# Optimization experiments

Measured on AMD Instinct MI355X. Metric: run time of the kernel, lower is better.

## Reference

```python
import jax, jax.numpy as jnp
import numpy as np

B, NF, E, A = 4096, 40, 64, 32  # batch, num feature fields, embedding_size, attention_size


def setup_inputs() -> dict:
    key = jax.random.key(0)
    kx, kw, kb, kh = jax.random.split(key, 4)
    return {
        "x": jax.random.normal(kx, (B, NF, E), dtype=jnp.float32),
        "W": jax.random.normal(kw, (E, A), dtype=jnp.float32) * 0.05,  # random_normal init
        "b": jax.random.normal(kb, (A,), dtype=jnp.float32) * 0.05,
        "h": jax.random.normal(kh, (A,), dtype=jnp.float32) * 0.05,
        "p": jnp.ones((E, 1), dtype=jnp.float32),  # 'ones' initializer
    }


def reference(x, W, b, h, p):
    nf = x.shape[1]
    # pairwise (i<j) element-wise products, same ordering as the double loop
    ii, jj = np.triu_indices(nf, k=1)
    ewp = x[:, ii, :] * x[:, jj, :]                      # (B, P, E), P = nf*(nf-1)/2
    # attention MLP: relu(ewp @ W + b) . h, then exp-normalize over pairs
    a = jax.nn.relu(jnp.einsum('bpe,ea->bpa', ewp, W) + b)  # (B, P, A)
    e = jnp.exp(jnp.sum(a * h, axis=-1))                 # (B, P)  (faithful: no max-subtract)
    att = e / jnp.sum(e, axis=1, keepdims=True)          # (B, P)
    pooled = jnp.einsum('bp,bpe->be', att, ewp)          # attention-weighted sum over pairs
    return pooled @ p                                    # (B, 1)
```

## Files before the change

kernel.cpp:

```cpp
#include <hip/hip_runtime.h>

#define NFEAT 40
#define EMB   64
#define ATT   32
#define NPAIR 780
#define NMT   49
#define XH_S  72

typedef __attribute__((ext_vector_type(8))) _Float16 f16x8;
typedef __attribute__((ext_vector_type(4))) _Float16 f16x4;
typedef __attribute__((ext_vector_type(4))) float    f32x4;

template <int CTRL>
__device__ __forceinline__ float dpp_add_f(float v) {
  int t = __builtin_amdgcn_update_dpp(0, __float_as_int(v), CTRL, 0xF, 0xF, true);
  return v + __int_as_float(t);
}
__device__ __forceinline__ float rowsum16(float v) {
  v = dpp_add_f<0x128>(v);
  v = dpp_add_f<0x124>(v);
  v = dpp_add_f<0x122>(v);
  v = dpp_add_f<0x121>(v);
  return v;
}

__device__ __forceinline__ int pair_off(int i) { return 39 * i - (i * (i - 1)) / 2; }

extern "C" __global__ __launch_bounds__(256)
void afm_kernel(const float* __restrict__ xg, const float* __restrict__ Wg,
                const float* __restrict__ bg, const float* __restrict__ hg,
                const float* __restrict__ pg, float* __restrict__ outg, int nbatch) {
  __shared__ __align__(16) _Float16 xh[NFEAT * XH_S];
  __shared__ float red[4][2];

  const int tid  = threadIdx.x;
  const int lane = tid & 63, wid = tid >> 6;
  const int l15  = lane & 15, hk = lane >> 4;

  f16x8 wf0[2], wf1[2], wf2[2];
#pragma unroll
  for (int kk = 0; kk < 2; kk++) {
    f16x8 r0, r1, r2;
#pragma unroll
    for (int t = 0; t < 8; t++) {
      int krow = kk * 32 + hk * 8 + t;
      r0[t] = (_Float16)Wg[krow * ATT + l15];
      r1[t] = (_Float16)Wg[krow * ATT + 16 + l15];
      _Float16 pv = (_Float16)pg[krow];
      r2[t] = (l15 == 0) ? pv : (_Float16)0.f;
    }
    wf0[kk] = r0; wf1[kk] = r1; wf2[kk] = r2;
  }
  const float4 b0 = *(const float4*)&bg[hk * 4];
  const float4 b1 = *(const float4*)&bg[16 + hk * 4];
  const float4 h0 = *(const float4*)&hg[hk * 4];
  const float4 h1 = *(const float4*)&hg[16 + hk * 4];

  unsigned pij[13];
#pragma unroll
  for (int t = 0; t < 13; t++) {
    int p = (wid + 4 * t) * 16 + l15;
    int i = 0, j = 0;
    if (p < NPAIR) {
      i = (int)((79.0f - sqrtf(6241.0f - 8.0f * (float)p)) * 0.5f);
      if (i < 0) i = 0;
      while (pair_off(i + 1) <= p) ++i;
      while (pair_off(i) > p) --i;
      j = i + 1 + (p - pair_off(i));
    }
    pij[t] = (unsigned)(i * 144 + hk * 16) | ((unsigned)(j * 144 + hk * 16) << 16);
  }

  const f32x4 kz = {0.f, 0.f, 0.f, 0.f};

  for (int it = 0; it < 2; it++) {
    const int bb = blockIdx.x * 2 + it;
    if (bb >= nbatch) break;

    const float4* xsrc = (const float4*)(xg + (size_t)bb * (NFEAT * EMB));
    for (int f = tid; f < NFEAT * EMB / 4; f += 256) {
      float4 v = xsrc[f];
      int row = f >> 4, c = (f & 15) * 4;
      f16x4 h4 = {(_Float16)v.x, (_Float16)v.y, (_Float16)v.z, (_Float16)v.w};
      *(f16x4*)&xh[row * XH_S + c] = h4;
    }
    __syncthreads();

    float sum_e = 0.f, sum_es = 0.f;
#pragma unroll
    for (int t = 0; t < 13; t++) {
      if (t < 12 || wid == 0) {
        const unsigned offi = pij[t] & 0xFFFFu;
        const unsigned offj = pij[t] >> 16;
        const f16x8 xi0 = *(const f16x8*)((const char*)xh + offi);
        const f16x8 xj0 = *(const f16x8*)((const char*)xh + offj);
        const f16x8 xi1 = *(const f16x8*)((const char*)xh + offi + 64);
        const f16x8 xj1 = *(const f16x8*)((const char*)xh + offj + 64);
        f16x8 af0 = xi0 * xj0;
        f16x8 af1 = xi1 * xj1;
        f32x4 acc0 = __builtin_amdgcn_mfma_f32_16x16x32_f16(wf0[0], af0, kz, 0, 0, 0);
        f32x4 acc1 = __builtin_amdgcn_mfma_f32_16x16x32_f16(wf1[0], af0, kz, 0, 0, 0);
        f32x4 acc2 = __builtin_amdgcn_mfma_f32_16x16x32_f16(wf2[0], af0, kz, 0, 0, 0);
        acc0 = __builtin_amdgcn_mfma_f32_16x16x32_f16(wf0[1], af1, acc0, 0, 0, 0);
        acc1 = __builtin_amdgcn_mfma_f32_16x16x32_f16(wf1[1], af1, acc1, 0, 0, 0);
        acc2 = __builtin_amdgcn_mfma_f32_16x16x32_f16(wf2[1], af1, acc2, 0, 0, 0);
        float va = fmaf(fmaxf(acc0[0] + b0.x, 0.f), h0.x,
                   fmaf(fmaxf(acc0[1] + b0.y, 0.f), h0.y,
                   fmaf(fmaxf(acc0[2] + b0.z, 0.f), h0.z,
                        fmaxf(acc0[3] + b0.w, 0.f) * h0.w)));
        float vb = fmaf(fmaxf(acc1[0] + b1.x, 0.f), h1.x,
                   fmaf(fmaxf(acc1[1] + b1.y, 0.f), h1.y,
                   fmaf(fmaxf(acc1[2] + b1.z, 0.f), h1.z,
                        fmaxf(acc1[3] + b1.w, 0.f) * h1.w)));
        float v = va + vb;
        v += __shfl_xor(v, 16, 64);
        v += __shfl_xor(v, 32, 64);
        float e = __expf(v);
        if (t == 12) e = (l15 < 12) ? e : 0.f;
        sum_e += e;
        sum_es = fmaf(e, acc2[0], sum_es);
      }
    }

    sum_e = rowsum16(sum_e);
    sum_e += __shfl_xor(sum_e, 16, 64);
    sum_e += __shfl_xor(sum_e, 32, 64);
    sum_es = rowsum16(sum_es);
    sum_es += __shfl_xor(sum_es, 16, 64);
    sum_es += __shfl_xor(sum_es, 32, 64);
    if (lane == 0) { red[wid][0] = sum_e; red[wid][1] = sum_es; }
    __syncthreads();
    if (tid == 0) {
      float Z = (red[0][0] + red[1][0] + red[2][0] + red[3][0]) * 0.25f;
      float S = red[0][1] + red[1][1] + red[2][1] + red[3][1];
      outg[bb] = S / Z;
    }
  }
}

extern "C" void kernel_launch(void* const* d_in, const int* in_sizes, int n_in,
                              void* d_out, int out_size, void* d_ws, size_t ws_size,
                              hipStream_t stream) {
  const float* xg = (const float*)d_in[0];
  const float* Wg = (const float*)d_in[1];
  const float* bg = (const float*)d_in[2];
  const float* hg = (const float*)d_in[3];
  const float* pg = (const float*)d_in[4];
  float* outg = (float*)d_out;
  const int Bn = in_sizes[0] / (NFEAT * EMB);
  const int nblk = (Bn + 1) / 2;
  afm_kernel<<<dim3(nblk), dim3(256), 0, stream>>>(xg, Wg, bg, hg, pg, outg, Bn);
}
```

Before: 39.82 us.

## Use single-wave blocks with LDS pair table and bias folded into MFMA

Each block now runs one 64-lane wave instead of four, and that wave loops over all 49 pair tiles per batch row. Per-lane pair offsets move from registers into a shared-memory table, and the bias is passed in as the MFMA accumulator init. The cross-wave shared reduction and its extra barrier go away, and the output divide is done directly by lane 0. In exchange there is less parallelism per block, since 2048 blocks of one wave each serialize 49 tiles of work, plus an extra LDS read per tile.

Result: no change. 40.35 us (+1.3%).

```diff
diff --git a/kernel.cpp b/kernel.cpp
--- a/kernel.cpp
+++ b/kernel.cpp
@@ -4,7 +4,7 @@
 #define EMB   64
 #define ATT   32
 #define NPAIR 780
-#define NMT   49
+#define NTILE 49
 #define XH_S  72
 
 typedef __attribute__((ext_vector_type(8))) _Float16 f16x8;
@@ -26,16 +26,28 @@
 
 __device__ __forceinline__ int pair_off(int i) { return 39 * i - (i * (i - 1)) / 2; }
 
-extern "C" __global__ __launch_bounds__(256)
+extern "C" __global__ __launch_bounds__(64)
 void afm_kernel(const float* __restrict__ xg, const float* __restrict__ Wg,
                 const float* __restrict__ bg, const float* __restrict__ hg,
                 const float* __restrict__ pg, float* __restrict__ outg, int nbatch) {
   __shared__ __align__(16) _Float16 xh[NFEAT * XH_S];
-  __shared__ float red[4][2];
+  __shared__ unsigned prt[NTILE * 16];
 
-  const int tid  = threadIdx.x;
-  const int lane = tid & 63, wid = tid >> 6;
+  const int lane = threadIdx.x;
   const int l15  = lane & 15, hk = lane >> 4;
+  const unsigned hkoff = hk * 16;
+
+  for (int p = lane; p < NTILE * 16; p += 64) {
+    int i = 0, j = 0;
+    if (p < NPAIR) {
+      i = (int)((79.0f - sqrtf(6241.0f - 8.0f * (float)p)) * 0.5f);
+      if (i < 0) i = 0;
+      while (pair_off(i + 1) <= p) ++i;
+      while (pair_off(i) > p) --i;
+      j = i + 1 + (p - pair_off(i));
+    }
+    prt[p] = (unsigned)(i * 144) | ((unsigned)(j * 144) << 16);
+  }
 
   f16x8 wf0[2], wf1[2], wf2[2];
 #pragma unroll
@@ -53,23 +65,10 @@
   }
   const float4 b0 = *(const float4*)&bg[hk * 4];
   const float4 b1 = *(const float4*)&bg[16 + hk * 4];
+  const f32x4 cb0 = {b0.x, b0.y, b0.z, b0.w};
+  const f32x4 cb1 = {b1.x, b1.y, b1.z, b1.w};
   const float4 h0 = *(const float4*)&hg[hk * 4];
   const float4 h1 = *(const float4*)&hg[16 + hk * 4];
-
-  unsigned pij[13];
-#pragma unroll
-  for (int t = 0; t < 13; t++) {
-    int p = (wid + 4 * t) * 16 + l15;
-    int i = 0, j = 0;
-    if (p < NPAIR) {
-      i = (int)((79.0f - sqrtf(6241.0f - 8.0f * (float)p)) * 0.5f);
-      if (i < 0) i = 0;
-      while (pair_off(i + 1) <= p) ++i;
-      while (pair_off(i) > p) --i;
-      j = i + 1 + (p - pair_off(i));
-    }
-    pij[t] = (unsigned)(i * 144 + hk * 16) | ((unsigned)(j * 144 + hk * 16) << 16);
-  }
 
   const f32x4 kz = {0.f, 0.f, 0.f, 0.f};
 
@@ -78,7 +77,8 @@
     if (bb >= nbatch) break;
 
     const float4* xsrc = (const float4*)(xg + (size_t)bb * (NFEAT * EMB));
-    for (int f = tid; f < NFEAT * EMB / 4; f += 256) {
+#pragma unroll
+    for (int f = lane; f < NFEAT * EMB / 4; f += 64) {
       float4 v = xsrc[f];
       int row = f >> 4, c = (f & 15) * 4;
       f16x4 h4 = {(_Float16)v.x, (_Float16)v.y, (_Float16)v.z, (_Float16)v.w};
@@ -87,54 +87,43 @@
     __syncthreads();
 
     float sum_e = 0.f, sum_es = 0.f;
-#pragma unroll
-    for (int t = 0; t < 13; t++) {
-      if (t < 12 || wid == 0) {
-        const unsigned offi = pij[t] & 0xFFFFu;
-        const unsigned offj = pij[t] >> 16;
-        const f16x8 xi0 = *(const f16x8*)((const char*)xh + offi);
-        const f16x8 xj0 = *(const f16x8*)((const char*)xh + offj);
-        const f16x8 xi1 = *(const f16x8*)((const char*)xh + offi + 64);
-        const f16x8 xj1 = *(const f16x8*)((const char*)xh + offj + 64);
-        f16x8 af0 = xi0 * xj0;
-        f16x8 af1 = xi1 * xj1;
-        f32x4 acc0 = __builtin_amdgcn_mfma_f32_16x16x32_f16(wf0[0], af0, kz, 0, 0, 0);
-        f32x4 acc1 = __builtin_amdgcn_mfma_f32_16x16x32_f16(wf1[0], af0, kz, 0, 0, 0);
-        f32x4 acc2 = __builtin_amdgcn_mfma_f32_16x16x32_f16(wf2[0], af0, kz, 0, 0, 0);
-        acc0 = __builtin_amdgcn_mfma_f32_16x16x32_f16(wf0[1], af1, acc0, 0, 0, 0);
-        acc1 = __builtin_amdgcn_mfma_f32_16x16x32_f16(wf1[1], af1, acc1, 0, 0, 0);
-        acc2 = __builtin_amdgcn_mfma_f32_16x16x32_f16(wf2[1], af1, acc2, 0, 0, 0);
-        float va = fmaf(fmaxf(acc0[0] + b0.x, 0.f), h0.x,
-                   fmaf(fmaxf(acc0[1] + b0.y, 0.f), h0.y,
-                   fmaf(fmaxf(acc0[2] + b0.z, 0.f), h0.z,
-                        fmaxf(acc0[3] + b0.w, 0.f) * h0.w)));
-        float vb = fmaf(fmaxf(acc1[0] + b1.x, 0.f), h1.x,
-                   fmaf(fmaxf(acc1[1] + b1.y, 0.f), h1.y,
-                   fmaf(fmaxf(acc1[2] + b1.z, 0.f), h1.z,
-                        fmaxf(acc1[3] + b1.w, 0.f) * h1.w)));
-        float v = va + vb;
-        v += __shfl_xor(v, 16, 64);
-        v += __shfl_xor(v, 32, 64);
-        float e = __expf(v);
-        if (t == 12) e = (l15 < 12) ? e : 0.f;
-        sum_e += e;
-        sum_es = fmaf(e, acc2[0], sum_es);
-      }
+#pragma unroll 4
+    for (int t = 0; t < NTILE; t++) {
+      const unsigned pij = prt[t * 16 + l15];
+      const unsigned offi = (pij & 0xFFFFu) + hkoff;
+      const unsigned offj = (pij >> 16) + hkoff;
+      const f16x8 xi0 = *(const f16x8*)((const char*)xh + offi);
+      const f16x8 xj0 = *(const f16x8*)((const char*)xh + offj);
+      const f16x8 xi1 = *(const f16x8*)((const char*)xh + offi + 64);
+      const f16x8 xj1 = *(const f16x8*)((const char*)xh + offj + 64);
+      f16x8 af0 = xi0 * xj0;
+      f16x8 af1 = xi1 * xj1;
+      f32x4 acc0 = __builtin_amdgcn_mfma_f32_16x16x32_f16(wf0[0], af0, cb0, 0, 0, 0);
+      f32x4 acc1 = __builtin_amdgcn_mfma_f32_16x16x32_f16(wf1[0], af0, cb1, 0, 0, 0);
+      f32x4 acc2 = __builtin_amdgcn_mfma_f32_16x16x32_f16(wf2[0], af0, kz, 0, 0, 0);
+      acc0 = __builtin_amdgcn_mfma_f32_16x16x32_f16(wf0[1], af1, acc0, 0, 0, 0);
+      acc1 = __builtin_amdgcn_mfma_f32_16x16x32_f16(wf1[1], af1, acc1, 0, 0, 0);
+      acc2 = __builtin_amdgcn_mfma_f32_16x16x32_f16(wf2[1], af1, acc2, 0, 0, 0);
+      float va = fmaf(fmaxf(acc0[0], 0.f), h0.x,
+                 fmaf(fmaxf(acc0[1], 0.f), h0.y,
+                 fmaf(fmaxf(acc0[2], 0.f), h0.z,
+                      fmaxf(acc0[3], 0.f) * h0.w)));
+      float vb = fmaf(fmaxf(acc1[0], 0.f), h1.x,
+                 fmaf(fmaxf(acc1[1], 0.f), h1.y,
+                 fmaf(fmaxf(acc1[2], 0.f), h1.z,
+                      fmaxf(acc1[3], 0.f) * h1.w)));
+      float v = va + vb;
+      v += __shfl_xor(v, 16, 64);
+      v += __shfl_xor(v, 32, 64);
+      float e = (t * 16 + l15 < NPAIR) ? __expf(v) : 0.f;
+      sum_e += e;
+      sum_es = fmaf(e, acc2[0], sum_es);
     }
 
-    sum_e = rowsum16(sum_e);
-    sum_e += __shfl_xor(sum_e, 16, 64);
-    sum_e += __shfl_xor(sum_e, 32, 64);
+    sum_e  = rowsum16(sum_e);
     sum_es = rowsum16(sum_es);
-    sum_es += __shfl_xor(sum_es, 16, 64);
-    sum_es += __shfl_xor(sum_es, 32, 64);
-    if (lane == 0) { red[wid][0] = sum_e; red[wid][1] = sum_es; }
+    if (lane == 0) outg[bb] = sum_es / sum_e;
     __syncthreads();
-    if (tid == 0) {
-      float Z = (red[0][0] + red[1][0] + red[2][0] + red[3][0]) * 0.25f;
-      float S = red[0][1] + red[1][1] + red[2][1] + red[3][1];
-      outg[bb] = S / Z;
-    }
   }
 }
 
@@ -149,5 +138,5 @@
   float* outg = (float*)d_out;
   const int Bn = in_sizes[0] / (NFEAT * EMB);
   const int nblk = (Bn + 1) / 2;
-  afm_kernel<<<dim3(nblk), dim3(256), 0, stream>>>(xg, Wg, bg, hg, pg, outg, Bn);
+  afm_kernel<<<dim3(nblk), dim3(64), 0, stream>>>(xg, Wg, bg, hg, pg, outg, Bn);
 }
```
